# Optimization experiments

Measured on AMD Instinct MI355X. Metric: run time of the kernel, lower is better.

The kernel has to match this reference:

```python
import jax, jax.numpy as jnp
import numpy as np

N = 262144            # number of particles
H0 = 0.006            # base SPH support radius (unit square domain)
GRID = 256            # static upper bound on cells per dimension (actual ~170)
NUM_CELLS = GRID * GRID
K = 32                # max particles stored per cell (avg occupancy ~9.4)
NCAND = 9 * K         # searchRadius=1 -> 3x3 cell stencil
MAX_NEIGHBORS = 64    # padded neighbor-list width (avg neighbor count ~27)


def setup_inputs() -> dict:
    key = jax.random.key(0)
    kp, ks = jax.random.split(key)
    positions = jax.random.uniform(kp, (N, 2), dtype=jnp.float32)
    # supports in [0.9*H0, H0], mimicking mildly adaptive SPH supports
    supports = H0 * (0.9 + 0.1 * jax.random.uniform(ks, (N,), dtype=jnp.float32))
    return {"positions": positions, "supports": supports}


def _cell_linear_indices(positions, supports):
    # mirrors sortPositions: cell size = hMax, indices = ceil((p - qMin)/hMax)
    hMax = jnp.max(supports)
    qMin = jnp.min(positions, axis=0) - hMax
    ij = jnp.ceil((positions - qMin) / hMax).astype(jnp.int32)  # >= 1 by construction
    ij = jnp.clip(ij, 0, GRID - 1)
    return ij[:, 0] + GRID * ij[:, 1]


def _build_cell_table(lin):
    # dense equivalent of the hash-grid: sort by cell, counting-sort into [cell, slot]
    order = jnp.argsort(lin)                       # == sortingIndices in the original
    lin_s = lin[order]
    counts = jax.ops.segment_sum(jnp.ones(N, jnp.int32), lin, num_segments=NUM_CELLS)
    starts = jnp.cumsum(counts) - counts           # exclusive prefix sum == cumCell
    rank = jnp.arange(N, dtype=jnp.int32) - starts[lin_s].astype(jnp.int32)
    ovf = rank >= K                                # overflow slots -> dump row
    cell_t = jnp.where(ovf, NUM_CELLS, lin_s)
    slot_t = jnp.where(ovf, 0, rank)
    table = jnp.full((NUM_CELLS + 1, K), -1, dtype=jnp.int32)
    table = table.at[cell_t, slot_t].set(order.astype(jnp.int32))
    return table


def reference(positions, supports):
    lin = _cell_linear_indices(positions, supports)
    table = _build_cell_table(lin)

    # 3x3 stencil of neighbor cells (searchRadius = 1)
    dx, dy = jnp.meshgrid(jnp.arange(-1, 2), jnp.arange(-1, 2), indexing='ij')
    offs = (dx + GRID * dy).reshape(1, 9).astype(jnp.int32)
    cand_cells = jnp.clip(lin[:, None] + offs, 0, NUM_CELLS)  # [N, 9]

    cand = table[cand_cells].reshape(N, NCAND)     # [N, 288] candidate particle ids
    present = cand >= 0
    cidx = jnp.where(present, cand, 0)
    cpos = positions[cidx]                         # [N, 288, 2] gather (memory bound)
    diff = cpos - positions[:, None, :]
    dist = jnp.sqrt(jnp.sum(diff * diff, axis=-1)) # [N, 288]
    valid = present & (dist <= supports[:, None])  # |x_i - x_j| <= h_i (self included)
    count = jnp.sum(valid, axis=1).astype(jnp.int32)

    # compact valid candidates to the front, pad to MAX_NEIGHBORS
    order2 = jnp.argsort(jnp.where(valid, 0, 1).astype(jnp.int32), axis=1, stable=True)
    sel = order2[:, :MAX_NEIGHBORS]
    nbr = jnp.take_along_axis(cidx, sel, axis=1)
    dsel = jnp.take_along_axis(dist, sel, axis=1)
    inb = jnp.arange(MAX_NEIGHBORS)[None, :] < count[:, None]
    neighbors = jnp.where(inb, nbr, -1)
    radial = jnp.where(inb, dsel / supports[:, None], 0.0)  # fluidRadialDistances
    return neighbors, count, radial
```

## Files before the change

kernel.cpp:

```cpp
#include <hip/hip_runtime.h>
#include <float.h>

#define N_PART 262144
#define GRID_DIM 256
#define NUM_CELLS (GRID_DIM * GRID_DIM)
#define KP 32
#define MAXNB 64


__global__ __launch_bounds__(256) void prep_kernel(
        const float2* __restrict__ pos2, const float* __restrict__ sup,
        int* __restrict__ counts,
        float* __restrict__ bMinX, float* __restrict__ bMinY,
        float* __restrict__ bMaxH) {
    __shared__ unsigned s_minx, s_miny, s_maxh;
    int t = threadIdx.x, b = blockIdx.x;
    int tid = b * 256 + t;
    if (tid <= NUM_CELLS) counts[tid] = 0;
    if (t == 0) { s_minx = 0x7f7fffffu; s_miny = 0x7f7fffffu; s_maxh = 0u; }
    __syncthreads();
    float2 p = pos2[tid];
    float  h = sup[tid];
    atomicMin(&s_minx, __float_as_uint(p.x));
    atomicMin(&s_miny, __float_as_uint(p.y));
    atomicMax(&s_maxh, __float_as_uint(h));
    __syncthreads();
    if (t == 0) {
        bMinX[b] = __uint_as_float(s_minx);
        bMinY[b] = __uint_as_float(s_miny);
        bMaxH[b] = __uint_as_float(s_maxh);
    }
}

__global__ __launch_bounds__(256) void bin_kernel(
        const float2* __restrict__ pos2,
        const float* __restrict__ bMinX, const float* __restrict__ bMinY,
        const float* __restrict__ bMaxH,
        int* __restrict__ counts, int* __restrict__ tableA) {
    __shared__ unsigned s_minx, s_miny, s_maxh;
    int t = threadIdx.x;
    int tid = blockIdx.x * 256 + t;
    if (t == 0) { s_minx = 0x7f7fffffu; s_miny = 0x7f7fffffu; s_maxh = 0u; }
    __syncthreads();
    {
        float mx = FLT_MAX, my = FLT_MAX, mh = 0.0f;
        for (int k = t; k < 1024; k += 256) {
            mx = fminf(mx, bMinX[k]);
            my = fminf(my, bMinY[k]);
            mh = fmaxf(mh, bMaxH[k]);
        }
        atomicMin(&s_minx, __float_as_uint(mx));
        atomicMin(&s_miny, __float_as_uint(my));
        atomicMax(&s_maxh, __float_as_uint(mh));
    }
    __syncthreads();
    float hmax  = __uint_as_float(s_maxh);
    float qminx = __uint_as_float(s_minx) - hmax;
    float qminy = __uint_as_float(s_miny) - hmax;
    float2 p = pos2[tid];
    int cx = (int)ceilf((p.x - qminx) / hmax);
    int cy = (int)ceilf((p.y - qminy) / hmax);
    cx = min(max(cx, 0), GRID_DIM - 1);
    cy = min(max(cy, 0), GRID_DIM - 1);
    int c = cx + GRID_DIM * cy;
    int slot = atomicAdd(&counts[c], 1);
    if (slot < KP) tableA[(c << 5) + slot] = tid;
}

__global__ __launch_bounds__(256) void rank_kernel(
        const float2* __restrict__ pos2, const float* __restrict__ sup,
        const int* __restrict__ counts, const int* __restrict__ tableA,
        float4* __restrict__ Qpad) {
    int tid = blockIdx.x * 256 + threadIdx.x;
    int c   = tid >> 3;
    int s0  = tid & 7;
    int cnt = min(counts[c], KP);
    const int* row = tableA + (c << 5);
    for (int sl = s0; sl < cnt; sl += 8) {
        int id = row[sl];
        int rank = 0;
        for (int k = 0; k < cnt; k++) rank += (row[k] < id);
        float2 p = pos2[id];
        float  h = sup[id];
        float  hn  = __int_as_float(__float_as_int(h) + 1);
        double mid = 0.5 * ((double)h + (double)hn);
        double t2  = mid * mid;
        float  S   = (float)t2;
        S = ((double)S > t2) ? __int_as_float(__float_as_int(S) - 1) : S;
        Qpad[(c << 5) + rank] = make_float4(p.x, p.y, __int_as_float(id), S);
    }
}

__global__ __launch_bounds__(256) void query_kernel(
        const int* __restrict__ counts, const float4* __restrict__ Qpad,
        float* __restrict__ outN, float* __restrict__ outC,
        float* __restrict__ outR) {
#pragma clang fp contract(off)
    __shared__ int   s_id[4][MAXNB];
    __shared__ float s_s2[4][MAXNB];

    int t    = threadIdx.x;
    int lane = t & 63;
    int wsl  = t >> 6;
    int bid  = blockIdx.x;
    int swz  = (bid & 7) * (int)(gridDim.x >> 3) + (bid >> 3);
    int cell = __builtin_amdgcn_readfirstlane(swz * 4 + wsl);

    const int offs[9] = {-257, -1, 255, -256, 0, 256, -255, 1, 257};
    int cum[10], delta[9];
    cum[0] = 0;
#pragma unroll
    for (int o = 0; o < 9; o++) {
        int cl = min(max(cell + offs[o], 0), NUM_CELLS);
        int cc = min(__builtin_amdgcn_readfirstlane(counts[cl]), KP);
        delta[o]   = (cl << 5) - cum[o];
        cum[o + 1] = cum[o] + cc;
    }
    int T   = cum[9];
    int cnt = cum[5] - cum[4];
    if (cnt == 0) return;

    if (T <= 64) {
        int dsel = delta[0];
#pragma unroll
        for (int m = 1; m < 9; m++)
            dsel = (lane >= cum[m]) ? delta[m] : dsel;
        float4 q = Qpad[lane + dsel];
        unsigned long long maskT = (T >= 64) ? ~0ull : ((1ull << T) - 1ull);
        for (int s = 0; s < cnt; s++) {
            int src = cum[4] + s;
            float px = __int_as_float(__builtin_amdgcn_readlane(__float_as_int(q.x), src));
            float py = __int_as_float(__builtin_amdgcn_readlane(__float_as_int(q.y), src));
            int   ib = __builtin_amdgcn_readlane(__float_as_int(q.z), src);
            float S  = __int_as_float(__builtin_amdgcn_readlane(__float_as_int(q.w), src));
            float dx = q.x - px;
            float dy = q.y - py;
            float s2 = dx * dx + dy * dy;
            bool keep = (s2 <= S) && (lane < T);
            unsigned long long bal = __ballot(s2 <= S) & maskT;
            int rank = __builtin_amdgcn_mbcnt_hi(
                (unsigned)(bal >> 32),
                __builtin_amdgcn_mbcnt_lo((unsigned)bal, 0));
            if (keep) {
                s_id[wsl][rank] = __float_as_int(q.z);
                s_s2[wsl][rank] = s2;
            }
            int total = (int)__popcll(bal);
            int   jj = s_id[wsl][lane];
            float ss = s_s2[wsl][lane];
            bool inb = lane < total;
            float rh = __builtin_amdgcn_rsqf(S);
            float vN = inb ? (float)jj : -1.0f;
            float vR = inb ? __builtin_amdgcn_sqrtf(ss) * rh : 0.0f;
            size_t base = (size_t)ib * MAXNB;
            outN[base + lane] = vN;
            outR[base + lane] = vR;
            if (lane == 0) outC[ib] = (float)total;
        }
    } else {
        for (int s = 0; s < cnt; s++) {
            float4 me = Qpad[(cell << 5) + s];
            int   ib = __builtin_amdgcn_readfirstlane(__float_as_int(me.z));
            float px = __int_as_float(__builtin_amdgcn_readfirstlane(__float_as_int(me.x)));
            float py = __int_as_float(__builtin_amdgcn_readfirstlane(__float_as_int(me.y)));
            float S  = __int_as_float(__builtin_amdgcn_readfirstlane(__float_as_int(me.w)));
            int total = 0;
            for (int b0 = 0; b0 < T; b0 += 64) {
                int ll = b0 + lane;
                int dsel = delta[0];
#pragma unroll
                for (int m = 1; m < 9; m++)
                    dsel = (ll >= cum[m]) ? delta[m] : dsel;
                float4 q = Qpad[ll + dsel];
                float dx = q.x - px;
                float dy = q.y - py;
                float s2 = dx * dx + dy * dy;
                int rem = T - b0;
                unsigned long long maskT =
                    (rem >= 64) ? ~0ull : ((1ull << rem) - 1ull);
                unsigned long long bal = __ballot(s2 <= S) & maskT;
                int rank = __builtin_amdgcn_mbcnt_hi(
                    (unsigned)(bal >> 32),
                    __builtin_amdgcn_mbcnt_lo((unsigned)bal, 0));
                int w = total + rank;
                if ((s2 <= S) && (ll < T) && (w < MAXNB)) {
                    s_id[wsl][w] = __float_as_int(q.z);
                    s_s2[wsl][w] = s2;
                }
                total += (int)__popcll(bal);
            }
            int stored = min(total, MAXNB);
            int   jj = s_id[wsl][lane];
            float ss = s_s2[wsl][lane];
            bool inb = lane < stored;
            float rh = __builtin_amdgcn_rsqf(S);
            float vN = inb ? (float)jj : -1.0f;
            float vR = inb ? __builtin_amdgcn_sqrtf(ss) * rh : 0.0f;
            size_t base = (size_t)ib * MAXNB;
            outN[base + lane] = vN;
            outR[base + lane] = vR;
            if (lane == 0) outC[ib] = (float)total;
        }
    }
}

extern "C" void kernel_launch(void* const* d_in, const int* in_sizes, int n_in,
                              void* d_out, int out_size, void* d_ws, size_t ws_size,
                              hipStream_t stream) {
    const float2* pos2 = (const float2*)d_in[0];
    const float*  sup  = (const float*)d_in[1];

    char* p = (char*)d_ws;
    auto alloc = [&](size_t bytes) {
        char* q = p;
        p += (bytes + 255) & ~(size_t)255;
        return q;
    };
    int*    counts = (int*)alloc((size_t)(NUM_CELLS + 1) * 4);
    float*  bMinX  = (float*)alloc(1024 * 4);
    float*  bMinY  = (float*)alloc(1024 * 4);
    float*  bMaxH  = (float*)alloc(1024 * 4);
    int*    tableA = (int*)alloc((size_t)(NUM_CELLS + 1) * KP * 4);
    float4* Qpad   = (float4*)alloc(((size_t)(NUM_CELLS + 1) * KP + 64) * 16);

    float* out  = (float*)d_out;
    float* outN = out;
    float* outC = out + (size_t)N_PART * MAXNB;
    float* outR = outC + N_PART;

    prep_kernel<<<N_PART / 256, 256, 0, stream>>>(pos2, sup, counts,
                                                  bMinX, bMinY, bMaxH);
    bin_kernel<<<N_PART / 256, 256, 0, stream>>>(pos2, bMinX, bMinY, bMaxH,
                                                 counts, tableA);
    rank_kernel<<<NUM_CELLS * 8 / 256, 256, 0, stream>>>(pos2, sup, counts,
                                                         tableA, Qpad);
    query_kernel<<<NUM_CELLS / 4, 256, 0, stream>>>(counts, Qpad,
                                                    outN, outC, outR);
}
```

Baseline: 270.6 us.

## Map one wavefront per particle in query kernel with precomputed cell prefix info

The query kernel now assigns one wavefront to each particle instead of each cell, removing the serial per-particle loop inside a cell. The rank kernel additionally records each particle's cell/slot location and precomputes per-cell 3x3 stencil prefix counts so the query kernel skips recomputing them from counts. This trades more waves and redundant candidate loads per cell for better load balance and latency hiding. Particles dropped by cell overflow get no linR entry.

```diff
diff --git a/kernel.cpp b/kernel.cpp
--- a/kernel.cpp
+++ b/kernel.cpp
@@ -70,7 +70,8 @@
 __global__ __launch_bounds__(256) void rank_kernel(
         const float2* __restrict__ pos2, const float* __restrict__ sup,
         const int* __restrict__ counts, const int* __restrict__ tableA,
-        float4* __restrict__ Qpad) {
+        float4* __restrict__ Qpad, int* __restrict__ linR,
+        int4* __restrict__ cinfo) {
     int tid = blockIdx.x * 256 + threadIdx.x;
     int c   = tid >> 3;
     int s0  = tid & 7;
@@ -88,11 +89,27 @@
         float  S   = (float)t2;
         S = ((double)S > t2) ? __int_as_float(__float_as_int(S) - 1) : S;
         Qpad[(c << 5) + rank] = make_float4(p.x, p.y, __int_as_float(id), S);
+        linR[id] = (c << 5) | rank;
+    }
+    if (s0 == 0) {
+        const int offs[9] = {-257, -1, 255, -256, 0, 256, -255, 1, 257};
+        int cum = 0;
+        int v[9];
+#pragma unroll
+        for (int o = 0; o < 9; o++) {
+            int cl = min(max(c + offs[o], 0), NUM_CELLS);
+            cum += min(counts[cl], KP);
+            v[o] = cum;
+        }
+        cinfo[c * 3 + 0] = make_int4(v[0], v[1], v[2], v[3]);
+        cinfo[c * 3 + 1] = make_int4(v[4], v[5], v[6], v[7]);
+        cinfo[c * 3 + 2] = make_int4(v[8], 0, 0, 0);
     }
 }
 
 __global__ __launch_bounds__(256) void query_kernel(
-        const int* __restrict__ counts, const float4* __restrict__ Qpad,
+        const int* __restrict__ linR, const int4* __restrict__ cinfo,
+        const float4* __restrict__ Qpad,
         float* __restrict__ outN, float* __restrict__ outC,
         float* __restrict__ outR) {
 #pragma clang fp contract(off)
@@ -104,103 +121,96 @@
     int wsl  = t >> 6;
     int bid  = blockIdx.x;
     int swz  = (bid & 7) * (int)(gridDim.x >> 3) + (bid >> 3);
-    int cell = __builtin_amdgcn_readfirstlane(swz * 4 + wsl);
+    int w    = __builtin_amdgcn_readfirstlane(swz * 4 + wsl);
+
+    int lr = __builtin_amdgcn_readfirstlane(linR[w]);
+    int c  = lr >> 5;
+
+    int4 ca = cinfo[c * 3 + 0];
+    int4 cb = cinfo[c * 3 + 1];
+    int4 cz = cinfo[c * 3 + 2];
+    float4 me = Qpad[lr];
+    float px = me.x, py = me.y, S = me.w;
 
     const int offs[9] = {-257, -1, 255, -256, 0, 256, -255, 1, 257};
-    int cum[10], delta[9];
-    cum[0] = 0;
+    int cum[10] = {0, ca.x, ca.y, ca.z, ca.w, cb.x, cb.y, cb.z, cb.w, };
+    cum[9] = cz.x;
+    int T = cum[9];
+    int delta[9];
 #pragma unroll
     for (int o = 0; o < 9; o++) {
-        int cl = min(max(cell + offs[o], 0), NUM_CELLS);
-        int cc = min(__builtin_amdgcn_readfirstlane(counts[cl]), KP);
-        delta[o]   = (cl << 5) - cum[o];
-        cum[o + 1] = cum[o] + cc;
-    }
-    int T   = cum[9];
-    int cnt = cum[5] - cum[4];
-    if (cnt == 0) return;
+        int cl = min(max(c + offs[o], 0), NUM_CELLS);
+        delta[o] = (cl << 5) - cum[o];
+    }
 
     if (T <= 64) {
         int dsel = delta[0];
 #pragma unroll
         for (int m = 1; m < 9; m++)
             dsel = (lane >= cum[m]) ? delta[m] : dsel;
-        float4 q = Qpad[lane + dsel];
+        int idx = (lane < T) ? (lane + dsel) : lr;
+        float4 q = Qpad[idx];
         unsigned long long maskT = (T >= 64) ? ~0ull : ((1ull << T) - 1ull);
-        for (int s = 0; s < cnt; s++) {
-            int src = cum[4] + s;
-            float px = __int_as_float(__builtin_amdgcn_readlane(__float_as_int(q.x), src));
-            float py = __int_as_float(__builtin_amdgcn_readlane(__float_as_int(q.y), src));
-            int   ib = __builtin_amdgcn_readlane(__float_as_int(q.z), src);
-            float S  = __int_as_float(__builtin_amdgcn_readlane(__float_as_int(q.w), src));
+        float dx = q.x - px;
+        float dy = q.y - py;
+        float s2 = dx * dx + dy * dy;
+        bool keep = (s2 <= S) && (lane < T);
+        unsigned long long bal = __ballot(s2 <= S) & maskT;
+        int rank = __builtin_amdgcn_mbcnt_hi(
+            (unsigned)(bal >> 32),
+            __builtin_amdgcn_mbcnt_lo((unsigned)bal, 0));
+        if (keep) {
+            s_id[wsl][rank] = __float_as_int(q.z);
+            s_s2[wsl][rank] = s2;
+        }
+        int total = (int)__popcll(bal);
+        int   jj = s_id[wsl][lane];
+        float ss = s_s2[wsl][lane];
+        bool inb = lane < total;
+        float rh = __builtin_amdgcn_rsqf(S);
+        float vN = inb ? (float)jj : -1.0f;
+        float vR = inb ? __builtin_amdgcn_sqrtf(ss) * rh : 0.0f;
+        size_t base = (size_t)w * MAXNB;
+        outN[base + lane] = vN;
+        outR[base + lane] = vR;
+        if (lane == 0) outC[w] = (float)total;
+    } else {
+        int total = 0;
+        for (int b0 = 0; b0 < T; b0 += 64) {
+            int ll = b0 + lane;
+            int dsel = delta[0];
+#pragma unroll
+            for (int m = 1; m < 9; m++)
+                dsel = (ll >= cum[m]) ? delta[m] : dsel;
+            float4 q = Qpad[ll + dsel];
             float dx = q.x - px;
             float dy = q.y - py;
             float s2 = dx * dx + dy * dy;
-            bool keep = (s2 <= S) && (lane < T);
+            int rem = T - b0;
+            unsigned long long maskT =
+                (rem >= 64) ? ~0ull : ((1ull << rem) - 1ull);
             unsigned long long bal = __ballot(s2 <= S) & maskT;
             int rank = __builtin_amdgcn_mbcnt_hi(
                 (unsigned)(bal >> 32),
                 __builtin_amdgcn_mbcnt_lo((unsigned)bal, 0));
-            if (keep) {
-                s_id[wsl][rank] = __float_as_int(q.z);
-                s_s2[wsl][rank] = s2;
+            int ww = total + rank;
+            if ((s2 <= S) && (ll < T) && (ww < MAXNB)) {
+                s_id[wsl][ww] = __float_as_int(q.z);
+                s_s2[wsl][ww] = s2;
             }
-            int total = (int)__popcll(bal);
-            int   jj = s_id[wsl][lane];
-            float ss = s_s2[wsl][lane];
-            bool inb = lane < total;
-            float rh = __builtin_amdgcn_rsqf(S);
-            float vN = inb ? (float)jj : -1.0f;
-            float vR = inb ? __builtin_amdgcn_sqrtf(ss) * rh : 0.0f;
-            size_t base = (size_t)ib * MAXNB;
-            outN[base + lane] = vN;
-            outR[base + lane] = vR;
-            if (lane == 0) outC[ib] = (float)total;
-        }
-    } else {
-        for (int s = 0; s < cnt; s++) {
-            float4 me = Qpad[(cell << 5) + s];
-            int   ib = __builtin_amdgcn_readfirstlane(__float_as_int(me.z));
-            float px = __int_as_float(__builtin_amdgcn_readfirstlane(__float_as_int(me.x)));
-            float py = __int_as_float(__builtin_amdgcn_readfirstlane(__float_as_int(me.y)));
-            float S  = __int_as_float(__builtin_amdgcn_readfirstlane(__float_as_int(me.w)));
-            int total = 0;
-            for (int b0 = 0; b0 < T; b0 += 64) {
-                int ll = b0 + lane;
-                int dsel = delta[0];
-#pragma unroll
-                for (int m = 1; m < 9; m++)
-                    dsel = (ll >= cum[m]) ? delta[m] : dsel;
-                float4 q = Qpad[ll + dsel];
-                float dx = q.x - px;
-                float dy = q.y - py;
-                float s2 = dx * dx + dy * dy;
-                int rem = T - b0;
-                unsigned long long maskT =
-                    (rem >= 64) ? ~0ull : ((1ull << rem) - 1ull);
-                unsigned long long bal = __ballot(s2 <= S) & maskT;
-                int rank = __builtin_amdgcn_mbcnt_hi(
-                    (unsigned)(bal >> 32),
-                    __builtin_amdgcn_mbcnt_lo((unsigned)bal, 0));
-                int w = total + rank;
-                if ((s2 <= S) && (ll < T) && (w < MAXNB)) {
-                    s_id[wsl][w] = __float_as_int(q.z);
-                    s_s2[wsl][w] = s2;
-                }
-                total += (int)__popcll(bal);
-            }
-            int stored = min(total, MAXNB);
-            int   jj = s_id[wsl][lane];
-            float ss = s_s2[wsl][lane];
-            bool inb = lane < stored;
-            float rh = __builtin_amdgcn_rsqf(S);
-            float vN = inb ? (float)jj : -1.0f;
-            float vR = inb ? __builtin_amdgcn_sqrtf(ss) * rh : 0.0f;
-            size_t base = (size_t)ib * MAXNB;
-            outN[base + lane] = vN;
-            outR[base + lane] = vR;
-            if (lane == 0) outC[ib] = (float)total;
-        }
+            total += (int)__popcll(bal);
+        }
+        int stored = min(total, MAXNB);
+        int   jj = s_id[wsl][lane];
+        float ss = s_s2[wsl][lane];
+        bool inb = lane < stored;
+        float rh = __builtin_amdgcn_rsqf(S);
+        float vN = inb ? (float)jj : -1.0f;
+        float vR = inb ? __builtin_amdgcn_sqrtf(ss) * rh : 0.0f;
+        size_t base = (size_t)w * MAXNB;
+        outN[base + lane] = vN;
+        outR[base + lane] = vR;
+        if (lane == 0) outC[w] = (float)total;
     }
 }
 
@@ -222,6 +232,8 @@
     float*  bMaxH  = (float*)alloc(1024 * 4);
     int*    tableA = (int*)alloc((size_t)(NUM_CELLS + 1) * KP * 4);
     float4* Qpad   = (float4*)alloc(((size_t)(NUM_CELLS + 1) * KP + 64) * 16);
+    int*    linR   = (int*)alloc((size_t)N_PART * 4);
+    int4*   cinfo  = (int4*)alloc((size_t)NUM_CELLS * 3 * 16);
 
     float* out  = (float*)d_out;
     float* outN = out;
@@ -233,7 +245,8 @@
     bin_kernel<<<N_PART / 256, 256, 0, stream>>>(pos2, bMinX, bMinY, bMaxH,
                                                  counts, tableA);
     rank_kernel<<<NUM_CELLS * 8 / 256, 256, 0, stream>>>(pos2, sup, counts,
-                                                         tableA, Qpad);
-    query_kernel<<<NUM_CELLS / 4, 256, 0, stream>>>(counts, Qpad,
-                                                    outN, outC, outR);
-}
+                                                         tableA, Qpad, linR,
+                                                         cinfo);
+    query_kernel<<<N_PART / 4, 256, 0, stream>>>(linR, cinfo, Qpad,
+                                                 outN, outC, outR);
+}
```

Result: no change. 267.4 us (-1.2%).
